# Performance work log

Measured on AMD Instinct MI355X. Metric: run time of the kernel, lower is better.

The kernel has to match this reference:

```python
import jax, jax.numpy as jnp
import numpy as np

B, N, M = 16, 2048, 2048


def setup_inputs() -> dict:
    key = jax.random.key(0)
    k1, k2, k3 = jax.random.split(key, 3)
    pred_dsmat = jax.random.uniform(k1, (B, N, M), dtype=jnp.float32)
    # valid sizes: src_ns <= tgt_ns so a permutation GT exists for every valid row
    src_ns = jax.random.randint(k2, (B,), 1024, 1537, dtype=jnp.int32)
    tgt_ns = jax.random.randint(k3, (B,), 1537, 2049, dtype=jnp.int32)
    # gt_perm: identity permutation restricted to the valid region (one 1 per valid row)
    i = jnp.arange(N)[:, None]
    j = jnp.arange(M)[None, :]
    eye = (i == j).astype(jnp.float32)  # [N, M]
    row_mask = (jnp.arange(N)[None, :] < src_ns[:, None]).astype(jnp.float32)  # [B, N]
    gt_perm = eye[None, :, :] * row_mask[:, :, None]  # [B, N, M]
    return {"pred_dsmat": pred_dsmat, "gt_perm": gt_perm,
            "src_ns": src_ns, "tgt_ns": tgt_ns, "beta_value": 0.1}


def reference(pred_dsmat, gt_perm, src_ns, tgt_ns, beta_value):
    Bn, Nn, Mn = pred_dsmat.shape
    row_mask = jnp.arange(Nn)[None, :] < src_ns[:, None]   # [B, N] bool
    col_mask = jnp.arange(Mn)[None, :] < tgt_ns[:, None]   # [B, M] bool
    mask = row_mask[:, :, None] & col_mask[:, None, :]     # [B, N, M]

    pred = jnp.clip(pred_dsmat, 0.0, 1.0) * mask
    gt = gt_perm * mask

    gt_pred = pred * gt                      # gt-selected predicted values
    row_gt = gt_pred.sum(axis=2)             # [B, N] per-row GT value
    col_gt = gt_pred.sum(axis=1)             # [B, M] per-col GT value
    row_cnt = gt.sum(axis=2)                 # [B, N] #GT matches per row
    col_cnt = gt.sum(axis=1)                 # [B, M] #GT matches per col

    # attention masks: entries >= (gt value - beta), restricted to valid region
    att_src = ((pred >= row_gt[:, :, None] - beta_value) & mask) * row_cnt[:, :, None]
    att_tgt = ((pred >= col_gt[:, None, :] - beta_value) & mask) * col_cnt[:, None, :]

    src_neg = jnp.sum(((att_src - gt) * pred) ** 2, axis=2)  # [B, N]
    src_pos = jnp.sum(gt_pred ** 2, axis=2)                  # [B, N]
    tgt_neg = jnp.sum(((att_tgt - gt) * pred) ** 2, axis=1)  # [B, M]

    # sum of tgt_neg over the GT-matched column of each row == dot with column counts
    corr = jnp.einsum('bm,bm->b', tgt_neg, col_cnt)          # [B]

    denom = 1.0 + src_neg + corr[:, None]                    # [B, N]
    num = jnp.where(row_mask, src_pos, 1.0)
    den = jnp.where(row_mask, denom, 1.0)
    loss = -0.5 * jnp.sum(jnp.log(num / den) * row_mask)
    n_sum = src_ns.sum().astype(pred.dtype)
    return loss / n_sum
```

## Files before the change

kernel.cpp:

```cpp
#include <hip/hip_runtime.h>

#define B_ 16
#define N_ 2048
#define M_ 2048
#define ROWS 32
#define WROWS 8
#define KCAP 2

__device__ __forceinline__ float wave_sum(float v) {
#pragma unroll
    for (int off = 32; off >= 1; off >>= 1) v += __shfl_xor(v, off);
    return v;
}

extern "C" __global__ __launch_bounds__(256) void k_pass1(
    const float* __restrict__ pred, const float* __restrict__ gt,
    const int* __restrict__ src_ns, const int* __restrict__ tgt_ns,
    const float* __restrict__ beta_p,
    float* __restrict__ col_gt, float* __restrict__ col_cnt,
    float* __restrict__ src_neg, float* __restrict__ src_pos,
    int* __restrict__ nnz, int* __restrict__ ent_col,
    float* __restrict__ ent_val, int* flag)
{
    const int b = blockIdx.y;
    const int src = src_ns[b];
    const int band = blockIdx.x;
    if (band * ROWS >= src) return;
    const int tgt = tgt_ns[b];
    const float beta = beta_p[0];
    const int wave = threadIdx.x >> 6, lane = threadIdx.x & 63;
    const int base = b * (N_ * M_);

    float4 acg[8], accn[8];
#pragma unroll
    for (int j = 0; j < 8; ++j) { acg[j] = make_float4(0,0,0,0); accn[j] = make_float4(0,0,0,0); }

    const int row0 = band * ROWS + wave * WROWS;
    for (int r = 0; r < WROWS; ++r) {
        const int n = row0 + r;
        if (n >= src) break;
        const int ri = b * N_ + n;
        const float4* prow = (const float4*)(pred + base + n * M_);
        const float4* grow = (const float4*)(gt + base + n * M_);
        float rg = 0.f, rc = 0.f;
        float4 pr[8], gr[8];
#pragma unroll
        for (int j = 0; j < 8; ++j) {
            const int m4 = j * 64 + lane;
            float4 p4 = prow[m4];
            float4 g4 = grow[m4];
            const int mb = m4 * 4;
#define P1C(KK, MB) do { \
    const int c = mb + KK; \
    const bool ok = c < tgt; \
    float p = fminf(fmaxf(p4.MB, 0.f), 1.f); p = ok ? p : 0.f; \
    const float gv = ok ? g4.MB : 0.f; \
    const float gp = p * gv; \
    rg += gp; rc += gv; \
    acg[j].MB += gp; accn[j].MB += gv; \
    p4.MB = p; g4.MB = gv; \
    if (gv != 0.f) { \
        const int slot = atomicAdd(&nnz[ri], 1); \
        if (slot < KCAP) { ent_col[ri * KCAP + slot] = c; ent_val[ri * KCAP + slot] = gv; } \
        else *flag = 1; \
    } \
} while (0)
            P1C(0, x); P1C(1, y); P1C(2, z); P1C(3, w);
#undef P1C
            pr[j] = p4; gr[j] = g4;
        }
        rg = wave_sum(rg); rc = wave_sum(rc);
        const float rth = rg - beta;
        float sneg = 0.f, spos = 0.f;
#pragma unroll
        for (int j = 0; j < 8; ++j) {
#define P1S(MB) do { \
    const float p = pr[j].MB; const float gv = gr[j].MB; \
    const float as = (p >= rth) ? rc : 0.f; \
    const float ds = (as - gv) * p; \
    sneg += ds * ds; \
    const float gp = gv * p; spos += gp * gp; \
} while (0)
            P1S(x); P1S(y); P1S(z); P1S(w);
#undef P1S
        }
        sneg = wave_sum(sneg); spos = wave_sum(spos);
        if (lane == 0) { src_neg[ri] = sneg; src_pos[ri] = spos; }
    }

    __shared__ float4 s_cg[M_ / 4];
    __shared__ float4 s_cc[M_ / 4];
    for (int i = threadIdx.x; i < M_ / 4; i += 256) {
        s_cg[i] = make_float4(0,0,0,0);
        s_cc[i] = make_float4(0,0,0,0);
    }
    __syncthreads();
    for (int w = 0; w < 4; ++w) {
        if (wave == w) {
#pragma unroll
            for (int j = 0; j < 8; ++j) {
                const int i = j * 64 + lane;
                float4 v = s_cg[i];
                v.x += acg[j].x; v.y += acg[j].y; v.z += acg[j].z; v.w += acg[j].w;
                s_cg[i] = v;
                float4 u = s_cc[i];
                u.x += accn[j].x; u.y += accn[j].y; u.z += accn[j].z; u.w += accn[j].w;
                s_cc[i] = u;
            }
        }
        __syncthreads();
    }
    const float* fcg = (const float*)s_cg;
    const float* fcc = (const float*)s_cc;
    for (int i = threadIdx.x; i < M_; i += 256) {
        atomicAdd(&col_gt[b * M_ + i], fcg[i]);
        atomicAdd(&col_cnt[b * M_ + i], fcc[i]);
    }
}

extern "C" __global__ __launch_bounds__(256) void k_pass2(
    const float* __restrict__ pred, const float* __restrict__ gt,
    const int* __restrict__ src_ns, const int* __restrict__ tgt_ns,
    const float* __restrict__ beta_p,
    const float* __restrict__ col_gt, const float* __restrict__ col_cnt,
    const int* __restrict__ nnz, const int* __restrict__ ent_col,
    const float* __restrict__ ent_val, const int* flag,
    float* __restrict__ tgt_neg)
{
    const int b = blockIdx.y;
    const int src = src_ns[b];
    const int band = blockIdx.x;
    if (band * ROWS >= src) return;
    const int tgt = tgt_ns[b];
    const float beta = beta_p[0];
    const int wave = threadIdx.x >> 6, lane = threadIdx.x & 63;
    const int base = b * (N_ * M_);
    const bool dense = (*flag != 0);

    float4 cg[8], cc[8], tn[8];
    const float4* cg4 = (const float4*)(col_gt + b * M_);
    const float4* cc4 = (const float4*)(col_cnt + b * M_);
#pragma unroll
    for (int j = 0; j < 8; ++j) {
        cg[j] = cg4[j * 64 + lane];
        cc[j] = cc4[j * 64 + lane];
        tn[j] = make_float4(0,0,0,0);
    }

    const int row0 = band * ROWS + wave * WROWS;
    if (!dense) {
        for (int r = 0; r < WROWS; ++r) {
            const int n = row0 + r;
            if (n >= src) break;
            const float4* prow = (const float4*)(pred + base + n * M_);
#pragma unroll
            for (int j = 0; j < 8; ++j) {
                const int m4 = j * 64 + lane;
                const float4 p4 = prow[m4];
                const int mb = m4 * 4;
#define P2S(KK, MB) do { \
    const bool ok = (mb + KK) < tgt; \
    float p = fminf(fmaxf(p4.MB, 0.f), 1.f); p = ok ? p : 0.f; \
    const float at = (p >= cg[j].MB - beta) ? cc[j].MB : 0.f; \
    const float d = at * p; \
    tn[j].MB += d * d; \
} while (0)
                P2S(0, x); P2S(1, y); P2S(2, z); P2S(3, w);
#undef P2S
            }
            const int ri = b * N_ + n;
            const int nn = nnz[ri];
            if (nn > 0 && lane == 0) {
                const int ne = nn < KCAP ? nn : KCAP;
                for (int s = 0; s < ne; ++s) {
                    const int c = ent_col[ri * KCAP + s];
                    const float gv = ent_val[ri * KCAP + s];
                    float pv = pred[base + n * M_ + c];
                    pv = fminf(fmaxf(pv, 0.f), 1.f);
                    const float at = (pv >= col_gt[b * M_ + c] - beta) ? col_cnt[b * M_ + c] : 0.f;
                    const float d0 = at * pv;
                    const float d1 = (at - gv) * pv;
                    atomicAdd(&tgt_neg[b * M_ + c], d1 * d1 - d0 * d0);
                }
            }
        }
    } else {
        for (int r = 0; r < WROWS; ++r) {
            const int n = row0 + r;
            if (n >= src) break;
            const float4* prow = (const float4*)(pred + base + n * M_);
            const float4* grow = (const float4*)(gt + base + n * M_);
#pragma unroll
            for (int j = 0; j < 8; ++j) {
                const int m4 = j * 64 + lane;
                const float4 p4 = prow[m4];
                const float4 g4 = grow[m4];
                const int mb = m4 * 4;
#define P2D(KK, MB) do { \
    const bool ok = (mb + KK) < tgt; \
    float p = fminf(fmaxf(p4.MB, 0.f), 1.f); p = ok ? p : 0.f; \
    const float gv = ok ? g4.MB : 0.f; \
    const float at = (ok && (p >= cg[j].MB - beta)) ? cc[j].MB : 0.f; \
    const float dt = (at - gv) * p; \
    tn[j].MB += dt * dt; \
} while (0)
                P2D(0, x); P2D(1, y); P2D(2, z); P2D(3, w);
#undef P2D
            }
        }
    }

    __shared__ float4 s_tn[M_ / 4];
    for (int i = threadIdx.x; i < M_ / 4; i += 256) s_tn[i] = make_float4(0,0,0,0);
    __syncthreads();
    for (int w = 0; w < 4; ++w) {
        if (wave == w) {
#pragma unroll
            for (int j = 0; j < 8; ++j) {
                const int i = j * 64 + lane;
                float4 v = s_tn[i];
                v.x += tn[j].x; v.y += tn[j].y; v.z += tn[j].z; v.w += tn[j].w;
                s_tn[i] = v;
            }
        }
        __syncthreads();
    }
    const float* ftn = (const float*)s_tn;
    for (int i = threadIdx.x; i < M_; i += 256)
        atomicAdd(&tgt_neg[b * M_ + i], ftn[i]);
}

extern "C" __global__ __launch_bounds__(256) void k_final(
    const float* __restrict__ src_neg, const float* __restrict__ src_pos,
    const float* __restrict__ tgt_neg, const float* __restrict__ col_cnt,
    const int* __restrict__ src_ns, float* __restrict__ out)
{
    const int b = blockIdx.x;
    const int wave = threadIdx.x >> 6, lane = threadIdx.x & 63;
    __shared__ float sredc[4];
    __shared__ float sredl[4];

    float c = 0.f;
    for (int i = threadIdx.x; i < M_; i += 256)
        c += tgt_neg[b * M_ + i] * col_cnt[b * M_ + i];
    c = wave_sum(c);
    if (lane == 0) sredc[wave] = c;
    __syncthreads();
    const float corr = sredc[0] + sredc[1] + sredc[2] + sredc[3];

    const int src = src_ns[b];
    float ls = 0.f;
    for (int n = threadIdx.x; n < src; n += 256) {
        const float sp = src_pos[b * N_ + n];
        const float sn = src_neg[b * N_ + n];
        ls += logf(sp) - logf(1.f + sn + corr);
    }
    ls = wave_sum(ls);
    if (lane == 0) sredl[wave] = ls;
    __syncthreads();
    if (threadIdx.x == 0) {
        const float total = sredl[0] + sredl[1] + sredl[2] + sredl[3];
        float nsum = 0.f;
        for (int i = 0; i < B_; ++i) nsum += (float)src_ns[i];
        atomicAdd(out, -0.5f * total / nsum);
    }
}

extern "C" void kernel_launch(void* const* d_in, const int* in_sizes, int n_in,
                              void* d_out, int out_size, void* d_ws, size_t ws_size,
                              hipStream_t stream)
{
    const float* pred   = (const float*)d_in[0];
    const float* gtp    = (const float*)d_in[1];
    const int*   src_ns = (const int*)d_in[2];
    const int*   tgt_ns = (const int*)d_in[3];
    const float* beta   = (const float*)d_in[4];
    float* out = (float*)d_out;
    float* ws  = (float*)d_ws;

    float* col_gt  = ws;
    float* col_cnt = col_gt  + B_ * M_;
    float* tgt_neg = col_cnt + B_ * M_;
    int*   nnz     = (int*)(tgt_neg + B_ * M_);
    int*   flag    = nnz + B_ * N_;
    float* src_neg = (float*)(flag + 1);
    float* src_pos = src_neg + B_ * N_;
    int*   ent_col = (int*)(src_pos + B_ * N_);
    float* ent_val = (float*)(ent_col + B_ * N_ * KCAP);

    const size_t zero_bytes = (size_t)(3 * B_ * M_ + B_ * N_ + 1) * sizeof(float);
    hipMemsetAsync(d_ws, 0, zero_bytes, stream);
    hipMemsetAsync(d_out, 0, sizeof(float), stream);

    dim3 grid(N_ / ROWS, B_);
    k_pass1<<<grid, 256, 0, stream>>>(pred, gtp, src_ns, tgt_ns, beta,
                                      col_gt, col_cnt, src_neg, src_pos,
                                      nnz, ent_col, ent_val, flag);
    k_pass2<<<grid, 256, 0, stream>>>(pred, gtp, src_ns, tgt_ns, beta,
                                      col_gt, col_cnt, nnz, ent_col, ent_val, flag,
                                      tgt_neg);
    k_final<<<B_, 256, 0, stream>>>(src_neg, src_pos, tgt_neg, col_cnt, src_ns, out);
}
```

Before: 567.2 us.

## Split pass into sparse GT scan, gather-based row/col sums, and single pred pass

Result: slower. 757.7 us (+33.6%).

```diff
diff --git a/kernel.cpp b/kernel.cpp
--- a/kernel.cpp
+++ b/kernel.cpp
@@ -5,7 +5,7 @@
 #define M_ 2048
 #define ROWS 32
 #define WROWS 8
-#define KCAP 2
+#define KCAP 4
 
 __device__ __forceinline__ float wave_sum(float v) {
 #pragma unroll
@@ -13,12 +13,9 @@
     return v;
 }
 
-extern "C" __global__ __launch_bounds__(256) void k_pass1(
-    const float* __restrict__ pred, const float* __restrict__ gt,
+extern "C" __global__ __launch_bounds__(256) void k_gt(
+    const float* __restrict__ gt,
     const int* __restrict__ src_ns, const int* __restrict__ tgt_ns,
-    const float* __restrict__ beta_p,
-    float* __restrict__ col_gt, float* __restrict__ col_cnt,
-    float* __restrict__ src_neg, float* __restrict__ src_pos,
     int* __restrict__ nnz, int* __restrict__ ent_col,
     float* __restrict__ ent_val, int* flag)
 {
@@ -27,65 +24,111 @@
     const int band = blockIdx.x;
     if (band * ROWS >= src) return;
     const int tgt = tgt_ns[b];
-    const float beta = beta_p[0];
     const int wave = threadIdx.x >> 6, lane = threadIdx.x & 63;
     const int base = b * (N_ * M_);
-
-    float4 acg[8], accn[8];
-#pragma unroll
-    for (int j = 0; j < 8; ++j) { acg[j] = make_float4(0,0,0,0); accn[j] = make_float4(0,0,0,0); }
+    const int jmax = (tgt + 255) >> 8;
 
     const int row0 = band * ROWS + wave * WROWS;
     for (int r = 0; r < WROWS; ++r) {
         const int n = row0 + r;
         if (n >= src) break;
         const int ri = b * N_ + n;
-        const float4* prow = (const float4*)(pred + base + n * M_);
         const float4* grow = (const float4*)(gt + base + n * M_);
-        float rg = 0.f, rc = 0.f;
-        float4 pr[8], gr[8];
-#pragma unroll
         for (int j = 0; j < 8; ++j) {
+            if (j >= jmax) break;
             const int m4 = j * 64 + lane;
-            float4 p4 = prow[m4];
-            float4 g4 = grow[m4];
-            const int mb = m4 * 4;
-#define P1C(KK, MB) do { \
+            const float4 g4 = grow[m4];
+            if (g4.x != 0.f || g4.y != 0.f || g4.z != 0.f || g4.w != 0.f) {
+                const int mb = m4 * 4;
+#define GC(KK, MB) do { \
     const int c = mb + KK; \
-    const bool ok = c < tgt; \
-    float p = fminf(fmaxf(p4.MB, 0.f), 1.f); p = ok ? p : 0.f; \
-    const float gv = ok ? g4.MB : 0.f; \
-    const float gp = p * gv; \
-    rg += gp; rc += gv; \
-    acg[j].MB += gp; accn[j].MB += gv; \
-    p4.MB = p; g4.MB = gv; \
-    if (gv != 0.f) { \
+    const float gv = g4.MB; \
+    if (gv != 0.f && c < tgt) { \
         const int slot = atomicAdd(&nnz[ri], 1); \
         if (slot < KCAP) { ent_col[ri * KCAP + slot] = c; ent_val[ri * KCAP + slot] = gv; } \
         else *flag = 1; \
     } \
 } while (0)
+                GC(0, x); GC(1, y); GC(2, z); GC(3, w);
+#undef GC
+            }
+        }
+    }
+}
+
+extern "C" __global__ __launch_bounds__(256) void k_mid(
+    const float* __restrict__ pred,
+    const int* __restrict__ src_ns,
+    const int* __restrict__ nnz, const int* __restrict__ ent_col,
+    const float* __restrict__ ent_val, const int* flag,
+    float* __restrict__ row_gt, float* __restrict__ row_cnt,
+    float* __restrict__ col_gt, float* __restrict__ col_cnt)
+{
+    if (*flag) return;
+    const int ri = blockIdx.x * 256 + threadIdx.x;
+    const int b = ri >> 11, n = ri & (N_ - 1);
+    if (n >= src_ns[b]) { row_gt[ri] = 0.f; row_cnt[ri] = 0.f; return; }
+    const int nn0 = nnz[ri];
+    const int nn = nn0 < KCAP ? nn0 : KCAP;
+    float rg = 0.f, rc = 0.f;
+    for (int s = 0; s < nn; ++s) {
+        const int c = ent_col[ri * KCAP + s];
+        const float gv = ent_val[ri * KCAP + s];
+        float p = pred[b * (N_ * M_) + n * M_ + c];
+        p = fminf(fmaxf(p, 0.f), 1.f);
+        rg += gv * p; rc += gv;
+        atomicAdd(&col_gt[b * M_ + c], gv * p);
+        atomicAdd(&col_cnt[b * M_ + c], gv);
+    }
+    row_gt[ri] = rg; row_cnt[ri] = rc;
+}
+
+extern "C" __global__ __launch_bounds__(256) void k_p1d(
+    const float* __restrict__ pred, const float* __restrict__ gt,
+    const int* __restrict__ src_ns, const int* __restrict__ tgt_ns,
+    const int* flag,
+    float* __restrict__ row_gt, float* __restrict__ row_cnt,
+    float* __restrict__ col_gt, float* __restrict__ col_cnt)
+{
+    if (*flag == 0) return;
+    const int b = blockIdx.y;
+    const int src = src_ns[b];
+    const int band = blockIdx.x;
+    if (band * ROWS >= src) return;
+    const int tgt = tgt_ns[b];
+    const int wave = threadIdx.x >> 6, lane = threadIdx.x & 63;
+    const int base = b * (N_ * M_);
+
+    float4 acg[8], accn[8];
+#pragma unroll
+    for (int j = 0; j < 8; ++j) { acg[j] = make_float4(0,0,0,0); accn[j] = make_float4(0,0,0,0); }
+
+    const int row0 = band * ROWS + wave * WROWS;
+    for (int r = 0; r < WROWS; ++r) {
+        const int n = row0 + r;
+        if (n >= src) break;
+        const float4* prow = (const float4*)(pred + base + n * M_);
+        const float4* grow = (const float4*)(gt + base + n * M_);
+        float rg = 0.f, rc = 0.f;
+#pragma unroll
+        for (int j = 0; j < 8; ++j) {
+            const int m4 = j * 64 + lane;
+            const float4 p4 = prow[m4];
+            const float4 g4 = grow[m4];
+            const int mb = m4 * 4;
+#define P1C(KK, MB) do { \
+    const bool ok = (mb + KK) < tgt; \
+    float p = fminf(fmaxf(p4.MB, 0.f), 1.f); p = ok ? p : 0.f; \
+    const float g = ok ? g4.MB : 0.f; \
+    const float gp = p * g; \
+    rg += gp; rc += g; \
+    acg[j].MB += gp; accn[j].MB += g; \
+} while (0)
             P1C(0, x); P1C(1, y); P1C(2, z); P1C(3, w);
 #undef P1C
-            pr[j] = p4; gr[j] = g4;
         }
         rg = wave_sum(rg); rc = wave_sum(rc);
-        const float rth = rg - beta;
-        float sneg = 0.f, spos = 0.f;
-#pragma unroll
-        for (int j = 0; j < 8; ++j) {
-#define P1S(MB) do { \
-    const float p = pr[j].MB; const float gv = gr[j].MB; \
-    const float as = (p >= rth) ? rc : 0.f; \
-    const float ds = (as - gv) * p; \
-    sneg += ds * ds; \
-    const float gp = gv * p; spos += gp * gp; \
-} while (0)
-            P1S(x); P1S(y); P1S(z); P1S(w);
-#undef P1S
-        }
-        sneg = wave_sum(sneg); spos = wave_sum(spos);
-        if (lane == 0) { src_neg[ri] = sneg; src_pos[ri] = spos; }
+        if (lane == 0) { row_gt[b * N_ + n] = rg; row_cnt[b * N_ + n] = rc; }
     }
 
     __shared__ float4 s_cg[M_ / 4];
@@ -118,13 +161,15 @@
     }
 }
 
-extern "C" __global__ __launch_bounds__(256) void k_pass2(
+extern "C" __global__ __launch_bounds__(256) void k_pred(
     const float* __restrict__ pred, const float* __restrict__ gt,
     const int* __restrict__ src_ns, const int* __restrict__ tgt_ns,
     const float* __restrict__ beta_p,
+    const float* __restrict__ row_gt, const float* __restrict__ row_cnt,
     const float* __restrict__ col_gt, const float* __restrict__ col_cnt,
     const int* __restrict__ nnz, const int* __restrict__ ent_col,
     const float* __restrict__ ent_val, const int* flag,
+    float* __restrict__ src_neg, float* __restrict__ src_pos,
     float* __restrict__ tgt_neg)
 {
     const int b = blockIdx.y;
@@ -136,13 +181,16 @@
     const int wave = threadIdx.x >> 6, lane = threadIdx.x & 63;
     const int base = b * (N_ * M_);
     const bool dense = (*flag != 0);
-
-    float4 cg[8], cc[8], tn[8];
+    const int jmax = (tgt + 255) >> 8;
+
+    float4 cgb[8], cc[8], tn[8];
     const float4* cg4 = (const float4*)(col_gt + b * M_);
     const float4* cc4 = (const float4*)(col_cnt + b * M_);
 #pragma unroll
     for (int j = 0; j < 8; ++j) {
-        cg[j] = cg4[j * 64 + lane];
+        float4 v = cg4[j * 64 + lane];
+        v.x -= beta; v.y -= beta; v.z -= beta; v.w -= beta;
+        cgb[j] = v;
         cc[j] = cc4[j * 64 + lane];
         tn[j] = make_float4(0,0,0,0);
     }
@@ -152,44 +200,62 @@
         for (int r = 0; r < WROWS; ++r) {
             const int n = row0 + r;
             if (n >= src) break;
+            const int ri = b * N_ + n;
+            const float rc = row_cnt[ri];
+            const float rth = row_gt[ri] - beta;
             const float4* prow = (const float4*)(pred + base + n * M_);
-#pragma unroll
+            float sneg = 0.f, spos = 0.f;
             for (int j = 0; j < 8; ++j) {
+                if (j >= jmax) break;
                 const int m4 = j * 64 + lane;
                 const float4 p4 = prow[m4];
                 const int mb = m4 * 4;
 #define P2S(KK, MB) do { \
     const bool ok = (mb + KK) < tgt; \
     float p = fminf(fmaxf(p4.MB, 0.f), 1.f); p = ok ? p : 0.f; \
-    const float at = (p >= cg[j].MB - beta) ? cc[j].MB : 0.f; \
+    const float as = (p >= rth) ? rc : 0.f; \
+    const float ds = as * p; \
+    sneg += ds * ds; \
+    const float at = (p >= cgb[j].MB) ? cc[j].MB : 0.f; \
     const float d = at * p; \
     tn[j].MB += d * d; \
 } while (0)
                 P2S(0, x); P2S(1, y); P2S(2, z); P2S(3, w);
 #undef P2S
             }
-            const int ri = b * N_ + n;
-            const int nn = nnz[ri];
-            if (nn > 0 && lane == 0) {
-                const int ne = nn < KCAP ? nn : KCAP;
-                for (int s = 0; s < ne; ++s) {
+            sneg = wave_sum(sneg);
+            if (lane == 0) {
+                const int nn0 = nnz[ri];
+                const int nn = nn0 < KCAP ? nn0 : KCAP;
+                for (int s = 0; s < nn; ++s) {
                     const int c = ent_col[ri * KCAP + s];
                     const float gv = ent_val[ri * KCAP + s];
                     float pv = pred[base + n * M_ + c];
                     pv = fminf(fmaxf(pv, 0.f), 1.f);
+                    const float as = (pv >= rth) ? rc : 0.f;
+                    const float d0 = as * pv;
+                    const float d1 = (as - gv) * pv;
+                    sneg += d1 * d1 - d0 * d0;
+                    const float gp = gv * pv;
+                    spos += gp * gp;
                     const float at = (pv >= col_gt[b * M_ + c] - beta) ? col_cnt[b * M_ + c] : 0.f;
-                    const float d0 = at * pv;
-                    const float d1 = (at - gv) * pv;
-                    atomicAdd(&tgt_neg[b * M_ + c], d1 * d1 - d0 * d0);
+                    const float t0 = at * pv;
+                    const float t1 = (at - gv) * pv;
+                    atomicAdd(&tgt_neg[b * M_ + c], t1 * t1 - t0 * t0);
                 }
+                src_neg[ri] = sneg; src_pos[ri] = spos;
             }
         }
     } else {
         for (int r = 0; r < WROWS; ++r) {
             const int n = row0 + r;
             if (n >= src) break;
+            const int ri = b * N_ + n;
+            const float rc = row_cnt[ri];
+            const float rth = row_gt[ri] - beta;
             const float4* prow = (const float4*)(pred + base + n * M_);
             const float4* grow = (const float4*)(gt + base + n * M_);
+            float sneg = 0.f, spos = 0.f;
 #pragma unroll
             for (int j = 0; j < 8; ++j) {
                 const int m4 = j * 64 + lane;
@@ -200,13 +266,19 @@
     const bool ok = (mb + KK) < tgt; \
     float p = fminf(fmaxf(p4.MB, 0.f), 1.f); p = ok ? p : 0.f; \
     const float gv = ok ? g4.MB : 0.f; \
-    const float at = (ok && (p >= cg[j].MB - beta)) ? cc[j].MB : 0.f; \
+    const float as = (p >= rth) ? rc : 0.f; \
+    const float ds = (as - gv) * p; \
+    sneg += ds * ds; \
+    const float gp = gv * p; spos += gp * gp; \
+    const float at = (p >= cgb[j].MB) ? cc[j].MB : 0.f; \
     const float dt = (at - gv) * p; \
     tn[j].MB += dt * dt; \
 } while (0)
                 P2D(0, x); P2D(1, y); P2D(2, z); P2D(3, w);
 #undef P2D
             }
+            sneg = wave_sum(sneg); spos = wave_sum(spos);
+            if (lane == 0) { src_neg[ri] = sneg; src_pos[ri] = spos; }
         }
     }
 
@@ -283,7 +355,9 @@
     float* tgt_neg = col_cnt + B_ * M_;
     int*   nnz     = (int*)(tgt_neg + B_ * M_);
     int*   flag    = nnz + B_ * N_;
-    float* src_neg = (float*)(flag + 1);
+    float* row_gt  = (float*)(flag + 1);
+    float* row_cnt = row_gt  + B_ * N_;
+    float* src_neg = row_cnt + B_ * N_;
     float* src_pos = src_neg + B_ * N_;
     int*   ent_col = (int*)(src_pos + B_ * N_);
     float* ent_val = (float*)(ent_col + B_ * N_ * KCAP);
@@ -293,11 +367,14 @@
     hipMemsetAsync(d_out, 0, sizeof(float), stream);
 
     dim3 grid(N_ / ROWS, B_);
-    k_pass1<<<grid, 256, 0, stream>>>(pred, gtp, src_ns, tgt_ns, beta,
-                                      col_gt, col_cnt, src_neg, src_pos,
-                                      nnz, ent_col, ent_val, flag);
-    k_pass2<<<grid, 256, 0, stream>>>(pred, gtp, src_ns, tgt_ns, beta,
-                                      col_gt, col_cnt, nnz, ent_col, ent_val, flag,
-                                      tgt_neg);
+    k_gt<<<grid, 256, 0, stream>>>(gtp, src_ns, tgt_ns, nnz, ent_col, ent_val, flag);
+    k_mid<<<(B_ * N_) / 256, 256, 0, stream>>>(pred, src_ns, nnz, ent_col, ent_val, flag,
+                                               row_gt, row_cnt, col_gt, col_cnt);
+    k_p1d<<<grid, 256, 0, stream>>>(pred, gtp, src_ns, tgt_ns, flag,
+                                    row_gt, row_cnt, col_gt, col_cnt);
+    k_pred<<<grid, 256, 0, stream>>>(pred, gtp, src_ns, tgt_ns, beta,
+                                     row_gt, row_cnt, col_gt, col_cnt,
+                                     nnz, ent_col, ent_val, flag,
+                                     src_neg, src_pos, tgt_neg);
     k_final<<<B_, 256, 0, stream>>>(src_neg, src_pos, tgt_neg, col_cnt, src_ns, out);
 }
```
